# Kernel tuning notes

Hardware: AMD Instinct MI355X
Metric: run time of the kernel (lower is better)

Reference implementation:

```python
import jax, jax.numpy as jnp
import numpy as np

B, S, D, H = 2, 2048, 1024, 16
DK = D // H


def setup_inputs() -> dict:
    key = jax.random.key(0)
    ks = jax.random.split(key, 12)
    scale = 1.0 / np.sqrt(D)
    inp = {
        "Q": jax.random.normal(ks[0], (B, S, D), jnp.float32),
        "K": jax.random.normal(ks[1], (B, S, D), jnp.float32),
        "V": jax.random.normal(ks[2], (B, S, D), jnp.float32),
        # causal mask, broadcast over batch: [B, S, S]
        "mask": jnp.broadcast_to(jnp.tril(jnp.ones((S, S), jnp.bool_)), (B, S, S)),
        "WQ_w": jax.random.normal(ks[3], (D, D), jnp.float32) * scale,
        "WQ_b": jnp.zeros((D,), jnp.float32),
        "WK_w": jax.random.normal(ks[4], (D, D), jnp.float32) * scale,
        "WK_b": jnp.zeros((D,), jnp.float32),
        "WV_w": jax.random.normal(ks[5], (D, D), jnp.float32) * scale,
        "WV_b": jnp.zeros((D,), jnp.float32),
        "WO_w": jax.random.normal(ks[6], (D, D), jnp.float32) * scale,
        "WO_b": jnp.zeros((D,), jnp.float32),
    }
    return inp


def reference(Q, K, V, mask, WQ_w, WQ_b, WK_w, WK_b, WV_w, WV_b, WO_w, WO_b):
    # Linear projections (torch Linear: x @ W.T + b), split heads -> [B,H,S,DK]
    def proj(x, w, b):
        return (x @ w.T + b).reshape(B, S, H, DK).transpose(0, 2, 1, 3)

    q = proj(Q, WQ_w, WQ_b)
    k = proj(K, WK_w, WK_b)
    v = proj(V, WV_w, WV_b)

    scores = jnp.einsum("bhqd,bhkd->bhqk", q, k) / jnp.sqrt(jnp.asarray(DK, q.dtype))
    scores = jnp.where(mask[:, None, :, :], scores, -jnp.inf)
    attn = jax.nn.softmax(scores, axis=-1)  # dropout is identity in eval mode

    out = jnp.einsum("bhqk,bhkd->bhqd", attn, v)
    out = out.transpose(0, 2, 1, 3).reshape(B, S, D)
    out = out @ WO_w.T + WO_b
    return (out, attn)
```

## Files before the change

kernel.cpp:

```cpp
#include <hip/hip_runtime.h>

#define S_LEN 2048
#define DMODEL 1024
#define NHEAD 16
#define DKH 64
#define BATCH 2

typedef __bf16 bf16_t;
typedef __bf16 bf16x8 __attribute__((ext_vector_type(8)));
typedef __bf16 bf16x4 __attribute__((ext_vector_type(4)));
typedef float f32x4 __attribute__((ext_vector_type(4)));

__device__ __forceinline__ void gload16(const bf16_t* g, bf16_t* l) {
  __builtin_amdgcn_global_load_lds(
      (const __attribute__((address_space(1))) unsigned int*)g,
      (__attribute__((address_space(3))) unsigned int*)l,
      16, 0, 0);
}

__global__ void cvt_all(const float* __restrict__ Q, const float* __restrict__ K,
                        const float* __restrict__ V, const float* __restrict__ WQ,
                        const float* __restrict__ WK, const float* __restrict__ WV,
                        const float* __restrict__ WO, bf16_t* __restrict__ dst) {
  const int i = blockIdx.x * 256 + threadIdx.x;
  const float* src;
  int off;
  if (i < 1572864) {
    const int seg = i >> 19;
    off = i & 524287;
    src = (seg == 0) ? Q : ((seg == 1) ? K : V);
  } else {
    const int j = i - 1572864;
    const int seg = j >> 17;
    off = j & 131071;
    src = (seg == 0) ? WQ : ((seg == 1) ? WK : ((seg == 2) ? WV : WO));
  }
  f32x4 a = *(const f32x4*)(src + (size_t)off * 8);
  f32x4 b = *(const f32x4*)(src + (size_t)off * 8 + 4);
  bf16x8 v;
#pragma unroll
  for (int j = 0; j < 4; ++j) { v[j] = (bf16_t)a[j]; v[4 + j] = (bf16_t)b[j]; }
  *(bf16x8*)(dst + (size_t)i * 8) = v;
}

struct GOp {
  const bf16_t* A;
  const bf16_t* W;
  const float* bias;
  char* out;
  int emode;
};

#define GM 4096
#define GN 1024
#define GK 1024
#define BM 128
#define BN 128
#define BK 64

__launch_bounds__(256, 3)
__global__ void gemm_bf16(GOp op0, GOp op1, GOp op2) {
  GOp op = (blockIdx.z == 0) ? op0 : ((blockIdx.z == 1) ? op1 : op2);
  const int n0 = blockIdx.x * BN;
  const int m0 = blockIdx.y * BM;
  const int t = threadIdx.x;
  const int w = t >> 6;
  const int l = t & 63;
  const int wr = w >> 1, wc = w & 1;
  const int lg = l >> 4, ll = l & 15;
  const int sr = l >> 3;
  const int sc = l & 7;

  __shared__ __align__(16) bf16_t Asm[BM * BK];
  __shared__ __align__(16) bf16_t Bsm[BM * BK];

  f32x4 acc[4][4] = {};

  for (int kt = 0; kt < GK / BK; ++kt) {
    __syncthreads();
#pragma unroll
    for (int i = 0; i < 4; ++i) {
      const int rbase = i * 32 + (w << 3);
      const int row = rbase + sr;
      const int gc = (sc ^ (row & 7)) << 3;
      gload16(op.A + (size_t)(m0 + row) * GK + kt * BK + gc, &Asm[rbase * BK]);
      gload16(op.W + (size_t)(n0 + row) * GK + kt * BK + gc, &Bsm[rbase * BK]);
    }
    __syncthreads();

    bf16x8 af[4][2], bfr[4][2];
#pragma unroll
    for (int mi = 0; mi < 4; ++mi) {
      const int row = wr * 64 + mi * 16 + ll;
      af[mi][0] = *(const bf16x8*)&Asm[row * BK + ((lg ^ (row & 7)) << 3)];
      af[mi][1] = *(const bf16x8*)&Asm[row * BK + (((4 + lg) ^ (row & 7)) << 3)];
    }
#pragma unroll
    for (int ni = 0; ni < 4; ++ni) {
      const int row = wc * 64 + ni * 16 + ll;
      bfr[ni][0] = *(const bf16x8*)&Bsm[row * BK + ((lg ^ (row & 7)) << 3)];
      bfr[ni][1] = *(const bf16x8*)&Bsm[row * BK + (((4 + lg) ^ (row & 7)) << 3)];
    }
#pragma unroll
    for (int mi = 0; mi < 4; ++mi)
#pragma unroll
      for (int ni = 0; ni < 4; ++ni) {
        acc[mi][ni] = __builtin_amdgcn_mfma_f32_16x16x32_bf16(af[mi][0], bfr[ni][0], acc[mi][ni], 0, 0, 0);
        acc[mi][ni] = __builtin_amdgcn_mfma_f32_16x16x32_bf16(af[mi][1], bfr[ni][1], acc[mi][ni], 0, 0, 0);
      }
  }

#pragma unroll
  for (int mi = 0; mi < 4; ++mi) {
#pragma unroll
    for (int ni = 0; ni < 4; ++ni) {
      const int col = n0 + wc * 64 + ni * 16 + ll;
      const int rbase = m0 + wr * 64 + mi * 16 + (lg << 2);
      const float bval = op.bias[col];
      f32x4 v = acc[mi][ni];
      if (op.emode == 0) {
        bf16_t* o = (bf16_t*)op.out;
#pragma unroll
        for (int r = 0; r < 4; ++r)
          o[(size_t)(rbase + r) * GN + col] = (bf16_t)(v[r] + bval);
      } else if (op.emode == 1) {
        const int hh = col >> 6, dd = col & 63;
        const int bb = rbase >> 11, ss = rbase & (S_LEN - 1);
        bf16_t* o = (bf16_t*)op.out + (((size_t)bb * NHEAD + hh) * DKH + dd) * S_LEN + ss;
        bf16x4 pk;
#pragma unroll
        for (int r = 0; r < 4; ++r) pk[r] = (bf16_t)(v[r] + bval);
        *(bf16x4*)o = pk;
      } else {
        float* o = (float*)op.out;
#pragma unroll
        for (int r = 0; r < 4; ++r)
          o[(size_t)(rbase + r) * GN + col] = v[r] + bval;
      }
    }
  }
}

__launch_bounds__(256, 3)
__global__ void attn2(const bf16_t* __restrict__ qp, const bf16_t* __restrict__ kp,
                      const bf16_t* __restrict__ vT, float* __restrict__ attn_out,
                      bf16_t* __restrict__ ctx) {
  const int raw = blockIdx.x;
  const int wg = (raw & 7) * 64 + (raw >> 3);
  const int bh = wg >> 4;
  const int pr = wg & 15;
  const int b = bh >> 4, h = bh & 15;
  const int flip = wg & 1;

  __shared__ __align__(16) bf16_t Qs[64 * 64];
  __shared__ __align__(16) bf16_t Ks[2][64 * 64];
  __shared__ __align__(16) bf16_t Vs[2][64 * 64];
  __shared__ __align__(16) bf16_t Pt[4][16 * 64];
  __shared__ float rinvS[64];

  const int t = threadIdx.x;
  const int w = t >> 6;
  const int l = t & 63;
  const int lg = l >> 4;
  const int ll = l & 15;
  const int sr = l >> 3;
  const int sc = l & 7;

  const bf16_t* kbh = kp + (size_t)b * S_LEN * DMODEL + h * DKH;
  const bf16_t* vbh = vT + (size_t)bh * DKH * S_LEN;

#define KV_STAGE(bu, kt)                                                           \
  {                                                                                \
    _Pragma("unroll") for (int i = 0; i < 2; ++i) {                                \
      const int rbase = i * 32 + (w << 3);                                         \
      const int row = rbase + sr;                                                  \
      const int gc = (sc ^ (row & 7)) << 3;                                        \
      gload16(kbh + (size_t)((kt) * 64 + row) * DMODEL + gc, &Ks[bu][rbase * 64]); \
      gload16(vbh + (size_t)row * S_LEN + (kt) * 64 + gc, &Vs[bu][rbase * 64]);    \
    }                                                                              \
  }

#define K_STAGE(bu, kt)                                                            \
  {                                                                                \
    _Pragma("unroll") for (int i = 0; i < 2; ++i) {                                \
      const int rbase = i * 32 + (w << 3);                                         \
      const int row = rbase + sr;                                                  \
      const int gc = (sc ^ (row & 7)) << 3;                                        \
      gload16(kbh + (size_t)((kt) * 64 + row) * DMODEL + gc, &Ks[bu][rbase * 64]); \
    }                                                                              \
  }

  for (int half = 0; half < 2; ++half) {
    const int qt = (half ^ flip) ? (31 - pr) : pr;
    const int q0 = qt * 64;
    const int nkt = qt + 1;

    __syncthreads();
#pragma unroll
    for (int i = 0; i < 2; ++i) {
      const int rbase = i * 32 + (w << 3);
      const int row = rbase + sr;
      const int gc = (sc ^ (row & 7)) << 3;
      gload16(qp + (size_t)(b * S_LEN + q0 + row) * DMODEL + h * DKH + gc, &Qs[rbase * 64]);
    }
    KV_STAGE(0, 0);
    __syncthreads();

    bf16x8 qf0, qf1;
    {
      const int row = w * 16 + ll;
      qf0 = *(const bf16x8*)&Qs[row * 64 + ((lg ^ (row & 7)) << 3)];
      qf1 = *(const bf16x8*)&Qs[row * 64 + (((4 + lg) ^ (row & 7)) << 3)];
    }

    f32x4 oacc[4] = {};
    float sums[4] = {0.f, 0.f, 0.f, 0.f};
    const int qrow_base = q0 + w * 16 + (lg << 2);

    int cur = 0;
    for (int kt = 0; kt < nkt; ++kt) {
      if (kt + 1 < nkt) KV_STAGE(cur ^ 1, kt + 1);

      const bool diag = (kt == qt);
#pragma unroll
      for (int cb = 0; cb < 4; ++cb) {
        const int krow = cb * 16 + ll;
        bf16x8 kf0 = *(const bf16x8*)&Ks[cur][krow * 64 + ((lg ^ (krow & 7)) << 3)];
        bf16x8 kf1 = *(const bf16x8*)&Ks[cur][krow * 64 + (((4 + lg) ^ (krow & 7)) << 3)];
        f32x4 a = {0.f, 0.f, 0.f, 0.f};
        a = __builtin_amdgcn_mfma_f32_16x16x32_bf16(qf0, kf0, a, 0, 0, 0);
        a = __builtin_amdgcn_mfma_f32_16x16x32_bf16(qf1, kf1, a, 0, 0, 0);
        const int gcol = kt * 64 + krow;
        if (diag) {
#pragma unroll
          for (int r = 0; r < 4; ++r) {
            const float e = (gcol <= qrow_base + r) ? __expf(a[r] * 0.125f) : 0.0f;
            sums[r] += e;
            const int ql = (lg << 2) + r;
            const int k = cb * 16 + ll;
            *(bf16_t*)((char*)&Pt[w][0] + ql * 128 + (((k >> 3) ^ (ql & 7)) << 4) + ((k & 7) << 1)) = (bf16_t)e;
          }
        } else {
#pragma unroll
          for (int r = 0; r < 4; ++r) {
            const float e = __expf(a[r] * 0.125f);
            sums[r] += e;
            const int ql = (lg << 2) + r;
            const int k = cb * 16 + ll;
            *(bf16_t*)((char*)&Pt[w][0] + ql * 128 + (((k >> 3) ^ (ql & 7)) << 4) + ((k & 7) << 1)) = (bf16_t)e;
          }
        }
      }
      bf16x8 pa0 = *(const bf16x8*)((char*)&Pt[w][0] + ll * 128 + ((lg ^ (ll & 7)) << 4));
      bf16x8 pa1 = *(const bf16x8*)((char*)&Pt[w][0] + ll * 128 + (((4 + lg) ^ (ll & 7)) << 4));
#pragma unroll
      for (int db = 0; db < 4; ++db) {
        const int drow = db * 16 + ll;
        bf16x8 vf0 = *(const bf16x8*)&Vs[cur][drow * 64 + ((lg ^ (drow & 7)) << 3)];
        bf16x8 vf1 = *(const bf16x8*)&Vs[cur][drow * 64 + (((4 + lg) ^ (drow & 7)) << 3)];
        oacc[db] = __builtin_amdgcn_mfma_f32_16x16x32_bf16(pa0, vf0, oacc[db], 0, 0, 0);
        oacc[db] = __builtin_amdgcn_mfma_f32_16x16x32_bf16(pa1, vf1, oacc[db], 0, 0, 0);
      }
      __syncthreads();
      cur ^= 1;
    }

    float rinv[4];
#pragma unroll
    for (int r = 0; r < 4; ++r) {
      float s = sums[r];
      s += __shfl_xor(s, 1);
      s += __shfl_xor(s, 2);
      s += __shfl_xor(s, 4);
      s += __shfl_xor(s, 8);
      rinv[r] = 1.0f / s;
    }
    if (ll == 0) {
#pragma unroll
      for (int r = 0; r < 4; ++r) rinvS[w * 16 + (lg << 2) + r] = rinv[r];
    }

    K_STAGE(0, 0);

#pragma unroll
    for (int db = 0; db < 4; ++db)
#pragma unroll
      for (int r = 0; r < 4; ++r) {
        const int grow = q0 + w * 16 + (lg << 2) + r;
        ctx[(size_t)(b * S_LEN + grow) * DMODEL + h * DKH + db * 16 + ll] = (bf16_t)(oacc[db][r] * rinv[r]);
      }
    __syncthreads();

    const float rv = rinvS[w * 16 + ll];
    float* arow = attn_out + ((size_t)bh * S_LEN + q0) * S_LEN;

    for (int kt = qt + 1; kt < 32; ++kt) {
      f32x4 z = {0.f, 0.f, 0.f, 0.f};
#pragma unroll
      for (int j = 0; j < 4; ++j) {
        const int row = w * 16 + (lg << 2) + j;
        *(f32x4*)(arow + (size_t)row * S_LEN + kt * 64 + (ll << 2)) = z;
      }
    }

    const int qrow_sw = q0 + w * 16 + ll;
    int cur2 = 0;
    for (int kt = 0; kt <= qt; ++kt) {
      if (kt + 1 <= qt) K_STAGE(cur2 ^ 1, kt + 1);

      const bool diag = (kt == qt);
#pragma unroll
      for (int i = 0; i < 4; ++i) {
        const int krow = i * 16 + ll;
        bf16x8 kf0 = *(const bf16x8*)&Ks[cur2][krow * 64 + ((lg ^ (krow & 7)) << 3)];
        bf16x8 kf1 = *(const bf16x8*)&Ks[cur2][krow * 64 + (((4 + lg) ^ (krow & 7)) << 3)];
        f32x4 a = {0.f, 0.f, 0.f, 0.f};
        a = __builtin_amdgcn_mfma_f32_16x16x32_bf16(kf0, qf0, a, 0, 0, 0);
        a = __builtin_amdgcn_mfma_f32_16x16x32_bf16(kf1, qf1, a, 0, 0, 0);
        const int kbase = kt * 64 + i * 16 + (lg << 2);
        f32x4 o;
        if (diag) {
#pragma unroll
          for (int r = 0; r < 4; ++r)
            o[r] = (kbase + r <= qrow_sw) ? __expf(a[r] * 0.125f) * rv : 0.0f;
        } else {
#pragma unroll
          for (int r = 0; r < 4; ++r) o[r] = __expf(a[r] * 0.125f) * rv;
        }
        *(f32x4*)(arow + (size_t)(w * 16 + ll) * S_LEN + kbase) = o;
      }
      __syncthreads();
      cur2 ^= 1;
    }
  }
#undef KV_STAGE
#undef K_STAGE
}

extern "C" void kernel_launch(void* const* d_in, const int* in_sizes, int n_in,
                              void* d_out, int out_size, void* d_ws, size_t ws_size,
                              hipStream_t stream) {
  const float* Q   = (const float*)d_in[0];
  const float* K   = (const float*)d_in[1];
  const float* V   = (const float*)d_in[2];
  const float* WQw = (const float*)d_in[4];
  const float* WQb = (const float*)d_in[5];
  const float* WKw = (const float*)d_in[6];
  const float* WKb = (const float*)d_in[7];
  const float* WVw = (const float*)d_in[8];
  const float* WVb = (const float*)d_in[9];
  const float* WOw = (const float*)d_in[10];
  const float* WOb = (const float*)d_in[11];

  char* ws = (char*)d_ws;
  bf16_t* qb  = (bf16_t*)(ws);
  bf16_t* kb  = (bf16_t*)(ws + (size_t)( 8 << 20));
  bf16_t* vb  = (bf16_t*)(ws + (size_t)(16 << 20));
  bf16_t* wq  = (bf16_t*)(ws + (size_t)(24 << 20));
  bf16_t* wk  = (bf16_t*)(ws + (size_t)(26 << 20));
  bf16_t* wv  = (bf16_t*)(ws + (size_t)(28 << 20));
  bf16_t* wo  = (bf16_t*)(ws + (size_t)(30 << 20));
  bf16_t* qp  = (bf16_t*)(ws + (size_t)(32 << 20));
  bf16_t* kp  = (bf16_t*)(ws + (size_t)(40 << 20));
  bf16_t* vT  = (bf16_t*)(ws + (size_t)(48 << 20));
  bf16_t* ctx = (bf16_t*)(ws + (size_t)(56 << 20));

  float* out_main = (float*)d_out;
  float* attn_out = out_main + (size_t)BATCH * S_LEN * DMODEL;

  cvt_all<<<dim3(8192), 256, 0, stream>>>(Q, K, V, WQw, WKw, WVw, WOw, (bf16_t*)ws);

  GOp opq{qb, wq, WQb, (char*)qp, 0};
  GOp opk{kb, wk, WKb, (char*)kp, 0};
  GOp opv{vb, wv, WVb, (char*)vT, 1};
  gemm_bf16<<<dim3(8, 32, 3), 256, 0, stream>>>(opq, opk, opv);

  attn2<<<dim3(512), 256, 0, stream>>>(qp, kp, vT, attn_out, ctx);

  GOp opo{ctx, wo, WOb, (char*)out_main, 2};
  gemm_bf16<<<dim3(8, 32, 1), 256, 0, stream>>>(opo, opo, opo);
}
```

Before: 229.4 us.

## Stage K/V in 128-row tiles to halve barriers in attention softmax pass

```diff
diff --git a/kernel.cpp b/kernel.cpp
--- a/kernel.cpp
+++ b/kernel.cpp
@@ -141,7 +141,7 @@
   }
 }
 
-__launch_bounds__(256, 3)
+__launch_bounds__(256, 2)
 __global__ void attn2(const bf16_t* __restrict__ qp, const bf16_t* __restrict__ kp,
                       const bf16_t* __restrict__ vT, float* __restrict__ attn_out,
                       bf16_t* __restrict__ ctx) {
@@ -153,10 +153,10 @@
   const int flip = wg & 1;
 
   __shared__ __align__(16) bf16_t Qs[64 * 64];
-  __shared__ __align__(16) bf16_t Ks[2][64 * 64];
-  __shared__ __align__(16) bf16_t Vs[2][64 * 64];
+  __shared__ __align__(16) bf16_t Ks[2][128 * 64];
+  __shared__ __align__(16) bf16_t Vs[2][2][64 * 64];
   __shared__ __align__(16) bf16_t Pt[4][16 * 64];
-  __shared__ float rinvS[64];
+  float* rinvS = (float*)&Pt[0][0];
 
   const int t = threadIdx.x;
   const int w = t >> 6;
@@ -169,15 +169,21 @@
   const bf16_t* kbh = kp + (size_t)b * S_LEN * DMODEL + h * DKH;
   const bf16_t* vbh = vT + (size_t)bh * DKH * S_LEN;
 
-#define KV_STAGE(bu, kt)                                                           \
-  {                                                                                \
-    _Pragma("unroll") for (int i = 0; i < 2; ++i) {                                \
-      const int rbase = i * 32 + (w << 3);                                         \
-      const int row = rbase + sr;                                                  \
-      const int gc = (sc ^ (row & 7)) << 3;                                        \
-      gload16(kbh + (size_t)((kt) * 64 + row) * DMODEL + gc, &Ks[bu][rbase * 64]); \
-      gload16(vbh + (size_t)row * S_LEN + (kt) * 64 + gc, &Vs[bu][rbase * 64]);    \
-    }                                                                              \
+#define KV_STAGE128(bu, ktt)                                                              \
+  {                                                                                       \
+    _Pragma("unroll") for (int i = 0; i < 4; ++i) {                                       \
+      const int rbase = i * 32 + (w << 3);                                                \
+      const int row = rbase + sr;                                                         \
+      const int gc = (sc ^ (row & 7)) << 3;                                               \
+      gload16(kbh + (size_t)((ktt) * 128 + row) * DMODEL + gc, &Ks[bu][rbase * 64]);      \
+    }                                                                                     \
+    _Pragma("unroll") for (int i = 0; i < 2; ++i) {                                       \
+      const int rbase = i * 32 + (w << 3);                                                \
+      const int row = rbase + sr;                                                         \
+      const int gc = (sc ^ (row & 7)) << 3;                                               \
+      gload16(vbh + (size_t)row * S_LEN + (ktt) * 128 + gc, &Vs[bu][0][rbase * 64]);      \
+      gload16(vbh + (size_t)row * S_LEN + (ktt) * 128 + 64 + gc, &Vs[bu][1][rbase * 64]); \
+    }                                                                                     \
   }
 
 #define K_STAGE(bu, kt)                                                            \
@@ -193,7 +199,7 @@
   for (int half = 0; half < 2; ++half) {
     const int qt = (half ^ flip) ? (31 - pr) : pr;
     const int q0 = qt * 64;
-    const int nkt = qt + 1;
+    const int nktt = (qt + 2) >> 1;
 
     __syncthreads();
 #pragma unroll
@@ -203,7 +209,7 @@
       const int gc = (sc ^ (row & 7)) << 3;
       gload16(qp + (size_t)(b * S_LEN + q0 + row) * DMODEL + h * DKH + gc, &Qs[rbase * 64]);
     }
-    KV_STAGE(0, 0);
+    KV_STAGE128(0, 0);
     __syncthreads();
 
     bf16x8 qf0, qf1;
@@ -218,48 +224,54 @@
     const int qrow_base = q0 + w * 16 + (lg << 2);
 
     int cur = 0;
-    for (int kt = 0; kt < nkt; ++kt) {
-      if (kt + 1 < nkt) KV_STAGE(cur ^ 1, kt + 1);
-
-      const bool diag = (kt == qt);
-#pragma unroll
-      for (int cb = 0; cb < 4; ++cb) {
-        const int krow = cb * 16 + ll;
-        bf16x8 kf0 = *(const bf16x8*)&Ks[cur][krow * 64 + ((lg ^ (krow & 7)) << 3)];
-        bf16x8 kf1 = *(const bf16x8*)&Ks[cur][krow * 64 + (((4 + lg) ^ (krow & 7)) << 3)];
-        f32x4 a = {0.f, 0.f, 0.f, 0.f};
-        a = __builtin_amdgcn_mfma_f32_16x16x32_bf16(qf0, kf0, a, 0, 0, 0);
-        a = __builtin_amdgcn_mfma_f32_16x16x32_bf16(qf1, kf1, a, 0, 0, 0);
-        const int gcol = kt * 64 + krow;
-        if (diag) {
-#pragma unroll
-          for (int r = 0; r < 4; ++r) {
-            const float e = (gcol <= qrow_base + r) ? __expf(a[r] * 0.125f) : 0.0f;
-            sums[r] += e;
-            const int ql = (lg << 2) + r;
-            const int k = cb * 16 + ll;
-            *(bf16_t*)((char*)&Pt[w][0] + ql * 128 + (((k >> 3) ^ (ql & 7)) << 4) + ((k & 7) << 1)) = (bf16_t)e;
+    for (int ktt = 0; ktt < nktt; ++ktt) {
+      if (ktt + 1 < nktt) KV_STAGE128(cur ^ 1, ktt + 1);
+
+#pragma unroll
+      for (int s = 0; s < 2; ++s) {
+        const int kk = 2 * ktt + s;
+        if (kk <= qt) {
+          const bool diag = (kk == qt);
+#pragma unroll
+          for (int cb = 0; cb < 4; ++cb) {
+            const int lr = s * 64 + cb * 16 + ll;
+            bf16x8 kf0 = *(const bf16x8*)&Ks[cur][lr * 64 + ((lg ^ (lr & 7)) << 3)];
+            bf16x8 kf1 = *(const bf16x8*)&Ks[cur][lr * 64 + (((4 + lg) ^ (lr & 7)) << 3)];
+            f32x4 a = {0.f, 0.f, 0.f, 0.f};
+            a = __builtin_amdgcn_mfma_f32_16x16x32_bf16(qf0, kf0, a, 0, 0, 0);
+            a = __builtin_amdgcn_mfma_f32_16x16x32_bf16(qf1, kf1, a, 0, 0, 0);
+            const int gcol = kk * 64 + cb * 16 + ll;
+            if (diag) {
+#pragma unroll
+              for (int r = 0; r < 4; ++r) {
+                const float e = (gcol <= qrow_base + r) ? __expf(a[r] * 0.125f) : 0.0f;
+                sums[r] += e;
+                const int ql = (lg << 2) + r;
+                const int k = cb * 16 + ll;
+                *(bf16_t*)((char*)&Pt[w][0] + ql * 128 + (((k >> 3) ^ (ql & 7)) << 4) + ((k & 7) << 1)) = (bf16_t)e;
+              }
+            } else {
+#pragma unroll
+              for (int r = 0; r < 4; ++r) {
+                const float e = __expf(a[r] * 0.125f);
+                sums[r] += e;
+                const int ql = (lg << 2) + r;
+                const int k = cb * 16 + ll;
+                *(bf16_t*)((char*)&Pt[w][0] + ql * 128 + (((k >> 3) ^ (ql & 7)) << 4) + ((k & 7) << 1)) = (bf16_t)e;
+              }
+            }
           }
-        } else {
-#pragma unroll
-          for (int r = 0; r < 4; ++r) {
-            const float e = __expf(a[r] * 0.125f);
-            sums[r] += e;
-            const int ql = (lg << 2) + r;
-            const int k = cb * 16 + ll;
-            *(bf16_t*)((char*)&Pt[w][0] + ql * 128 + (((k >> 3) ^ (ql & 7)) << 4) + ((k & 7) << 1)) = (bf16_t)e;
+          bf16x8 pa0 = *(const bf16x8*)((char*)&Pt[w][0] + ll * 128 + ((lg ^ (ll & 7)) << 4));
+          bf16x8 pa1 = *(const bf16x8*)((char*)&Pt[w][0] + ll * 128 + (((4 + lg) ^ (ll & 7)) << 4));
+#pragma unroll
+          for (int db = 0; db < 4; ++db) {
+            const int drow = db * 16 + ll;
+            bf16x8 vf0 = *(const bf16x8*)&Vs[cur][s][drow * 64 + ((lg ^ (drow & 7)) << 3)];
+            bf16x8 vf1 = *(const bf16x8*)&Vs[cur][s][drow * 64 + (((4 + lg) ^ (drow & 7)) << 3)];
+            oacc[db] = __builtin_amdgcn_mfma_f32_16x16x32_bf16(pa0, vf0, oacc[db], 0, 0, 0);
+            oacc[db] = __builtin_amdgcn_mfma_f32_16x16x32_bf16(pa1, vf1, oacc[db], 0, 0, 0);
           }
         }
-      }
-      bf16x8 pa0 = *(const bf16x8*)((char*)&Pt[w][0] + ll * 128 + ((lg ^ (ll & 7)) << 4));
-      bf16x8 pa1 = *(const bf16x8*)((char*)&Pt[w][0] + ll * 128 + (((4 + lg) ^ (ll & 7)) << 4));
-#pragma unroll
-      for (int db = 0; db < 4; ++db) {
-        const int drow = db * 16 + ll;
-        bf16x8 vf0 = *(const bf16x8*)&Vs[cur][drow * 64 + ((lg ^ (drow & 7)) << 3)];
-        bf16x8 vf1 = *(const bf16x8*)&Vs[cur][drow * 64 + (((4 + lg) ^ (drow & 7)) << 3)];
-        oacc[db] = __builtin_amdgcn_mfma_f32_16x16x32_bf16(pa0, vf0, oacc[db], 0, 0, 0);
-        oacc[db] = __builtin_amdgcn_mfma_f32_16x16x32_bf16(pa1, vf1, oacc[db], 0, 0, 0);
       }
       __syncthreads();
       cur ^= 1;
@@ -333,7 +345,7 @@
       cur2 ^= 1;
     }
   }
-#undef KV_STAGE
+#undef KV_STAGE128
 #undef K_STAGE
 }
 
```

Measured after the change: 225.1 us. About the same (-1.9%).

## Read K from global in attention-prob pass, drop LDS staging and barriers

Applied to the files above, without the earlier changes.

```diff
diff --git a/kernel.cpp b/kernel.cpp
--- a/kernel.cpp
+++ b/kernel.cpp
@@ -150,13 +150,13 @@
   const int bh = wg >> 4;
   const int pr = wg & 15;
   const int b = bh >> 4, h = bh & 15;
-  const int flip = wg & 1;
+  const int flip = (raw >> 8) & 1;
 
   __shared__ __align__(16) bf16_t Qs[64 * 64];
   __shared__ __align__(16) bf16_t Ks[2][64 * 64];
   __shared__ __align__(16) bf16_t Vs[2][64 * 64];
   __shared__ __align__(16) bf16_t Pt[4][16 * 64];
-  __shared__ float rinvS[64];
+  float* rinvS = (float*)&Pt[0][0];
 
   const int t = threadIdx.x;
   const int w = t >> 6;
@@ -168,26 +168,17 @@
 
   const bf16_t* kbh = kp + (size_t)b * S_LEN * DMODEL + h * DKH;
   const bf16_t* vbh = vT + (size_t)bh * DKH * S_LEN;
-
-#define KV_STAGE(bu, kt)                                                           \
-  {                                                                                \
-    _Pragma("unroll") for (int i = 0; i < 2; ++i) {                                \
-      const int rbase = i * 32 + (w << 3);                                         \
-      const int row = rbase + sr;                                                  \
-      const int gc = (sc ^ (row & 7)) << 3;                                        \
-      gload16(kbh + (size_t)((kt) * 64 + row) * DMODEL + gc, &Ks[bu][rbase * 64]); \
-      gload16(vbh + (size_t)row * S_LEN + (kt) * 64 + gc, &Vs[bu][rbase * 64]);    \
-    }                                                                              \
-  }
-
-#define K_STAGE(bu, kt)                                                            \
-  {                                                                                \
-    _Pragma("unroll") for (int i = 0; i < 2; ++i) {                                \
-      const int rbase = i * 32 + (w << 3);                                         \
-      const int row = rbase + sr;                                                  \
-      const int gc = (sc ^ (row & 7)) << 3;                                        \
-      gload16(kbh + (size_t)((kt) * 64 + row) * DMODEL + gc, &Ks[bu][rbase * 64]); \
-    }                                                                              \
+  const f32x4 zero4 = {0.f, 0.f, 0.f, 0.f};
+
+#define KV_STAGE(bu, kt_)                                                           \
+  {                                                                                 \
+    _Pragma("unroll") for (int i = 0; i < 2; ++i) {                                 \
+      const int rbase = i * 32 + (w << 3);                                          \
+      const int row = rbase + sr;                                                   \
+      const int gc = (sc ^ (row & 7)) << 3;                                         \
+      gload16(kbh + (size_t)((kt_) * 64 + row) * DMODEL + gc, &Ks[bu][rbase * 64]); \
+      gload16(vbh + (size_t)row * S_LEN + (kt_) * 64 + gc, &Vs[bu][rbase * 64]);    \
+    }                                                                               \
   }
 
   for (int half = 0; half < 2; ++half) {
@@ -222,6 +213,7 @@
       if (kt + 1 < nkt) KV_STAGE(cur ^ 1, kt + 1);
 
       const bool diag = (kt == qt);
+      __builtin_amdgcn_s_setprio(1);
 #pragma unroll
       for (int cb = 0; cb < 4; ++cb) {
         const int krow = cb * 16 + ll;
@@ -261,6 +253,7 @@
         oacc[db] = __builtin_amdgcn_mfma_f32_16x16x32_bf16(pa0, vf0, oacc[db], 0, 0, 0);
         oacc[db] = __builtin_amdgcn_mfma_f32_16x16x32_bf16(pa1, vf1, oacc[db], 0, 0, 0);
       }
+      __builtin_amdgcn_s_setprio(0);
       __syncthreads();
       cur ^= 1;
     }
@@ -280,8 +273,6 @@
       for (int r = 0; r < 4; ++r) rinvS[w * 16 + (lg << 2) + r] = rinv[r];
     }
 
-    K_STAGE(0, 0);
-
 #pragma unroll
     for (int db = 0; db < 4; ++db)
 #pragma unroll
@@ -289,31 +280,26 @@
         const int grow = q0 + w * 16 + (lg << 2) + r;
         ctx[(size_t)(b * S_LEN + grow) * DMODEL + h * DKH + db * 16 + ll] = (bf16_t)(oacc[db][r] * rinv[r]);
       }
-    __syncthreads();
 
     const float rv = rinvS[w * 16 + ll];
     float* arow = attn_out + ((size_t)bh * S_LEN + q0) * S_LEN;
 
     for (int kt = qt + 1; kt < 32; ++kt) {
-      f32x4 z = {0.f, 0.f, 0.f, 0.f};
 #pragma unroll
       for (int j = 0; j < 4; ++j) {
         const int row = w * 16 + (lg << 2) + j;
-        *(f32x4*)(arow + (size_t)row * S_LEN + kt * 64 + (ll << 2)) = z;
+        __builtin_nontemporal_store(zero4, (f32x4*)(arow + (size_t)row * S_LEN + kt * 64 + (ll << 2)));
       }
     }
 
     const int qrow_sw = q0 + w * 16 + ll;
-    int cur2 = 0;
     for (int kt = 0; kt <= qt; ++kt) {
-      if (kt + 1 <= qt) K_STAGE(cur2 ^ 1, kt + 1);
-
       const bool diag = (kt == qt);
 #pragma unroll
       for (int i = 0; i < 4; ++i) {
-        const int krow = i * 16 + ll;
-        bf16x8 kf0 = *(const bf16x8*)&Ks[cur2][krow * 64 + ((lg ^ (krow & 7)) << 3)];
-        bf16x8 kf1 = *(const bf16x8*)&Ks[cur2][krow * 64 + (((4 + lg) ^ (krow & 7)) << 3)];
+        const bf16_t* kp_ = kbh + (size_t)(kt * 64 + i * 16 + ll) * DMODEL + (lg << 3);
+        bf16x8 kf0 = *(const bf16x8*)kp_;
+        bf16x8 kf1 = *(const bf16x8*)(kp_ + 32);
         f32x4 a = {0.f, 0.f, 0.f, 0.f};
         a = __builtin_amdgcn_mfma_f32_16x16x32_bf16(kf0, qf0, a, 0, 0, 0);
         a = __builtin_amdgcn_mfma_f32_16x16x32_bf16(kf1, qf1, a, 0, 0, 0);
@@ -327,14 +313,11 @@
 #pragma unroll
           for (int r = 0; r < 4; ++r) o[r] = __expf(a[r] * 0.125f) * rv;
         }
-        *(f32x4*)(arow + (size_t)(w * 16 + ll) * S_LEN + kbase) = o;
-      }
-      __syncthreads();
-      cur2 ^= 1;
+        __builtin_nontemporal_store(o, (f32x4*)(arow + (size_t)(w * 16 + ll) * S_LEN + kbase));
+      }
     }
   }
 #undef KV_STAGE
-#undef K_STAGE
 }
 
 extern "C" void kernel_launch(void* const* d_in, const int* in_sizes, int n_in,
```

Result: slower. 250.6 us (+9.2%).
